# Performance work log

Measured on AMD Instinct MI355X. Metric: run time of the kernel, lower is better.

The kernel has to match this reference:

```python
import jax, jax.numpy as jnp
import numpy as np

EPS = 1e-7  # K.epsilon()
ROUTINGS = 3


def squash(s):
    # squash along last axis: s * ||s||^2 / (1 + ||s||^2) / ||s||
    sq_norm = jnp.sum(jnp.square(s), axis=-1, keepdims=True)
    scale = sq_norm / (1.0 + sq_norm) / jnp.sqrt(sq_norm + EPS)
    return scale * s


def setup_inputs() -> dict:
    key = jax.random.key(0)
    k1, k2 = jax.random.split(key)
    B, N, I = 64, 2048, 16      # batch, in_num_capsule, in_capsule_dim
    J, K = 32, 32               # num_capsule, capsule_dim
    inputs = jax.random.normal(k1, (B, N, I), dtype=jnp.float32)
    W = jax.random.normal(k2, (J, N, K, I), dtype=jnp.float32) * 0.05
    return {"inputs": inputs, "W": W}


def reference(inputs, W):
    # u_hat[b,j,n,k] = sum_i inputs[b,n,i] * W[j,n,k,i]
    u_hat = jnp.einsum('bni,jnki->bjnk', inputs, W)
    B, J, N, _ = u_hat.shape
    b = jnp.zeros((B, J, N), dtype=u_hat.dtype)
    outputs = None
    for i in range(ROUTINGS):
        c = jax.nn.softmax(b, axis=1)                       # softmax over num_capsule
        s = jnp.einsum('bjn,bjnk->bjk', c, u_hat)           # weighted sum over in caps
        outputs = squash(s)                                  # [B, J, K]
        if i < ROUTINGS - 1:
            b = b + jnp.einsum('bjk,bjnk->bjn', outputs, u_hat)
    return outputs
```

## Files before the change

kernel.cpp:

```cpp
#include <hip/hip_runtime.h>
#include <hip/hip_bf16.h>

typedef unsigned int  u32;
typedef unsigned short u16;
typedef __attribute__((ext_vector_type(8)))  short short8;
typedef __attribute__((ext_vector_type(16))) float f32x16;

#define B_ 64
#define N_ 2048
#define I_ 16
#define J_ 32
#define K_ 32
#define CH_  32
#define WTOT ((size_t)J_*N_*K_*I_)

__device__ __forceinline__ float bf2f(u16 u){ return __uint_as_float(((u32)u)<<16); }
__device__ __forceinline__ short f2bf(float f){
  __hip_bfloat16 h = __float2bfloat16(f);
  short s; __builtin_memcpy(&s, &h, 2); return s;
}

__global__ __launch_bounds__(256) void detect(const u16* __restrict__ X,
                                              const u16* __restrict__ W,
                                              int* __restrict__ flags)
{
  __shared__ int sx, sw;
  if (threadIdx.x == 0){ sx = 0; sw = 0; }
  __syncthreads();
  int bx = 0, bw = 0;
  for (int i = threadIdx.x; i < 8192; i += 256){
    int ex = (X[2*i] >> 7) & 0xFF;
    int ew = (W[2*i] >> 7) & 0xFF;
    if (ex >= 0x90) bx = 1;
    if (ew >= 0x90) bw = 1;
  }
  if (bx) atomicOr(&sx, 1);
  if (bw) atomicOr(&sw, 1);
  __syncthreads();
  if (threadIdx.x == 0){ flags[0] = sx; flags[1] = sw; }
}

__global__ __launch_bounds__(256) void pack_xw(const void* __restrict__ Xv,
                                               const void* __restrict__ Wv,
                                               const int* __restrict__ flags,
                                               u16* __restrict__ X_p,
                                               u16* __restrict__ W_p)
{
  if (blockIdx.x < 8192){
    const size_t base = ((size_t)blockIdx.x*256 + threadIdx.x)*16;
    if (flags[1]){
      const float4* src = (const float4*)((const float*)Wv + base);
      float4 v0=src[0], v1=src[1], v2=src[2], v3=src[3];
      short8 a, b;
      a[0]=f2bf(v0.x); a[1]=f2bf(v0.y); a[2]=f2bf(v0.z); a[3]=f2bf(v0.w);
      a[4]=f2bf(v1.x); a[5]=f2bf(v1.y); a[6]=f2bf(v1.z); a[7]=f2bf(v1.w);
      b[0]=f2bf(v2.x); b[1]=f2bf(v2.y); b[2]=f2bf(v2.z); b[3]=f2bf(v2.w);
      b[4]=f2bf(v3.x); b[5]=f2bf(v3.y); b[6]=f2bf(v3.z); b[7]=f2bf(v3.w);
      *(short8*)(W_p + base)     = a;
      *(short8*)(W_p + base + 8) = b;
    } else {
      const short8* src = (const short8*)((const u16*)Wv + base);
      *(short8*)(W_p + base)     = src[0];
      *(short8*)(W_p + base + 8) = src[1];
    }
  } else {
    const int bid = blockIdx.x - 8192;
    const int l = threadIdx.x & 63, w = threadIdx.x >> 6;
    const int n = bid*4 + w;
    const bool xf32 = flags[0] != 0;
    const int ih = (l>>5)*8;
    u16 out[16];
    #pragma unroll
    for (int t=0;t<2;++t){
      const int b = t*32 + (l&31);
      if (xf32){
        const float4* xp = (const float4*)((const float*)Xv + ((size_t)b*N_ + n)*I_ + ih);
        float4 v0 = xp[0], v1 = xp[1];
        out[t*8+0]=(u16)f2bf(v0.x); out[t*8+1]=(u16)f2bf(v0.y);
        out[t*8+2]=(u16)f2bf(v0.z); out[t*8+3]=(u16)f2bf(v0.w);
        out[t*8+4]=(u16)f2bf(v1.x); out[t*8+5]=(u16)f2bf(v1.y);
        out[t*8+6]=(u16)f2bf(v1.z); out[t*8+7]=(u16)f2bf(v1.w);
      } else {
        const u16* xp = (const u16*)Xv + ((size_t)b*N_ + n)*I_ + ih;
        #pragma unroll
        for (int q=0;q<8;++q) out[t*8+q] = xp[q];
      }
    }
    u16* dst = X_p + (size_t)n*1024 + l*16;
    short8 s0, s1;
    #pragma unroll
    for (int q=0;q<8;++q){ s0[q]=(short)out[q]; s1[q]=(short)out[8+q]; }
    *(short8*)dst = s0;
    *(short8*)(dst+8) = s1;
  }
}

template<int R>
__global__ __launch_bounds__(256) void accum_kernel(
    const u16* __restrict__ X_p, const u16* __restrict__ W_p,
    const float* __restrict__ c_buf, const float* __restrict__ sumb,
    float* __restrict__ part)
{
  __shared__ float red[4][2048];
  const int l  = threadIdx.x & 63;
  const int w  = threadIdx.x >> 6;
  const int j  = blockIdx.y;
  const int ch = blockIdx.x;
  const int n0 = ch*64 + w*16;
  const int kc = l & 31;
  const int ih = (l >> 5) * 8;

  f32x16 C0, C1;
  #pragma unroll
  for (int r=0;r<16;++r){ C0[r]=0.f; C1[r]=0.f; }

  #pragma unroll 4
  for (int t=0;t<16;++t){
    const int n = n0 + t;
    const u16* xp = X_p + (size_t)n*1024 + l*16;
    short8 xa0 = *(const short8*)xp;
    short8 xa1 = *(const short8*)(xp+8);
    short8 a0, a1;
    if constexpr (R==0){ a0 = xa0; a1 = xa1; }
    else {
      const float iS0 = sumb[(size_t)n*64 + kc];
      const float iS1 = sumb[(size_t)n*64 + 32 + kc];
      const float c0 = iS0 * c_buf[((size_t)n*J_ + j)*64 + kc];
      const float c1 = iS1 * c_buf[((size_t)n*J_ + j)*64 + 32 + kc];
      #pragma unroll
      for (int q=0;q<8;++q){
        a0[q] = f2bf(c0 * bf2f((u16)xa0[q]));
        a1[q] = f2bf(c1 * bf2f((u16)xa1[q]));
      }
    }
    short8 bfr = *(const short8*)(W_p + ((size_t)j*N_ + n)*512 + kc*16 + ih);
    C0 = __builtin_amdgcn_mfma_f32_32x32x16_bf16(a0, bfr, C0, 0,0,0);
    C1 = __builtin_amdgcn_mfma_f32_32x32x16_bf16(a1, bfr, C1, 0,0,0);
  }

  #pragma unroll
  for (int r=0;r<16;++r){
    red[w][r*64 + l]      = C0[r];
    red[w][(16+r)*64 + l] = C1[r];
  }
  __syncthreads();

  float* dst = part + ((size_t)ch*J_ + j)*2048;
  #pragma unroll
  for (int p = threadIdx.x; p < 2048; p += 256)
    dst[p] = red[0][p] + red[1][p] + red[2][p] + red[3][p];
}

template<int SQ>
__global__ __launch_bounds__(256) void reduce_squash(
    const float* __restrict__ part, float* __restrict__ o_t,
    const int* __restrict__ flags, void* __restrict__ d_out)
{
  const int j    = blockIdx.x & 31;
  const int rseg = blockIdx.x >> 5;
  const int rl   = threadIdx.x >> 6;
  const int l    = threadIdx.x & 63;
  const int r    = rseg*4 + rl;
  const int p    = r*64 + l;

  float sum = 0.f;
  const float* src = part + (size_t)j*2048 + p;
  #pragma unroll 8
  for (int ch=0; ch<CH_; ++ch)
    sum += src[(size_t)ch*J_*2048];

  const int kc = l & 31, h = l >> 5;
  const int rr = r & 15, tile = r >> 4;
  const int b  = tile*32 + (rr&3) + 8*(rr>>2) + 4*h;

  float v = sum;
  if constexpr (SQ==0) v *= (1.0f/32.0f);

  float sq = v*v;
  sq += __shfl_xor(sq, 1,  64);
  sq += __shfl_xor(sq, 2,  64);
  sq += __shfl_xor(sq, 4,  64);
  sq += __shfl_xor(sq, 8,  64);
  sq += __shfl_xor(sq, 16, 64);
  const float scale = sq/(1.f+sq)/sqrtf(sq+1e-7f);

  if constexpr (SQ==0){
    o_t[((size_t)j*K_ + kc)*64 + b] = scale * v;
  } else if constexpr (SQ==1){
    o_t[((size_t)j*K_ + kc)*64 + b] += scale * v;
  } else {
    const bool f32o = (flags[0]!=0) && (flags[1]!=0);
    if (f32o){
      ((float*)d_out)[(size_t)b*(J_*K_) + j*K_ + kc] = scale * v;
    } else {
      ((__hip_bfloat16*)d_out)[(size_t)b*(J_*K_) + j*K_ + kc] = __float2bfloat16(scale * v);
    }
  }
}

__global__ __launch_bounds__(256) void logits_kernel(
    const u16* __restrict__ X_p, const u16* __restrict__ W_p,
    const float* __restrict__ o_t, float* __restrict__ c_buf)
{
  const int l  = threadIdx.x & 63;
  const int w  = threadIdx.x >> 6;
  const int j  = blockIdx.y;
  const int n0 = blockIdx.x*32 + w*8;
  const int kc = l & 31;
  const int h  = l >> 5;
  const int ih = h*8;

  float o_r0[16], o_r1[16];
  #pragma unroll
  for (int r=0;r<16;++r){
    const int k = (r&3) + 8*(r>>2) + 4*h;
    o_r0[r] = o_t[((size_t)j*K_ + k)*64 + kc];
    o_r1[r] = o_t[((size_t)j*K_ + k)*64 + 32 + kc];
  }

  #pragma unroll 2
  for (int t=0;t<8;++t){
    const int n = n0 + t;
    const u16* xp = X_p + (size_t)n*1024 + l*16;
    short8 xa0 = *(const short8*)xp;
    short8 xa1 = *(const short8*)(xp+8);
    short8 wfr = *(const short8*)(W_p + ((size_t)j*N_ + n)*512 + kc*16 + ih);
    f32x16 C0, C1;
    #pragma unroll
    for (int r=0;r<16;++r){ C0[r]=0.f; C1[r]=0.f; }
    C0 = __builtin_amdgcn_mfma_f32_32x32x16_bf16(wfr, xa0, C0, 0,0,0);
    C1 = __builtin_amdgcn_mfma_f32_32x32x16_bf16(wfr, xa1, C1, 0,0,0);
    float d0 = 0.f, d1 = 0.f;
    #pragma unroll
    for (int r=0;r<16;++r){ d0 += C0[r]*o_r0[r]; d1 += C1[r]*o_r1[r]; }
    d0 += __shfl_xor(d0, 32, 64);
    d1 += __shfl_xor(d1, 32, 64);
    const float val = (l >= 32) ? d1 : d0;
    c_buf[((size_t)n*J_ + j)*64 + l] = __expf(val);
  }
}

__global__ __launch_bounds__(256) void rowsum(const float* __restrict__ c_buf,
                                              float* __restrict__ sumb)
{
  const int l = threadIdx.x & 63, w = threadIdx.x >> 6;
  const int n = blockIdx.x*4 + w;
  const float* p = c_buf + (size_t)n*J_*64 + l;
  float s = 0.f;
  #pragma unroll
  for (int jj=0;jj<J_;++jj) s += p[jj*64];
  sumb[(size_t)n*64 + l] = 1.0f/s;
}

extern "C" void kernel_launch(void* const* d_in, const int* in_sizes, int n_in,
                              void* d_out, int out_size, void* d_ws, size_t ws_size,
                              hipStream_t stream)
{
  const void* X  = d_in[0];
  const void* Wm = d_in[1];

  float* ws    = (float*)d_ws;
  float* o_t   = ws;
  int*   flags = (int*)(ws + 65536);
  u16*   X_p   = (u16*)(ws + 65536 + 128);
  u16*   W_p   = X_p + (size_t)N_*1024;
  float* c_buf = (float*)(W_p + WTOT);
  float* sumb  = c_buf + (size_t)N_*J_*64;
  float* part  = sumb + (size_t)N_*64;

  const dim3 blk(256);
  const dim3 g_ac(CH_, J_);
  const dim3 g_lg(64,  J_);

  detect<<<1, blk, 0, stream>>>((const u16*)X, (const u16*)Wm, flags);
  pack_xw<<<8192 + N_/4, blk, 0, stream>>>(X, Wm, flags, X_p, W_p);

  accum_kernel<0><<<g_ac, blk, 0, stream>>>(X_p, W_p, nullptr, nullptr, part);
  reduce_squash<0><<<256, blk, 0, stream>>>(part, o_t, flags, nullptr);

  logits_kernel<<<g_lg, blk, 0, stream>>>(X_p, W_p, o_t, c_buf);
  rowsum<<<N_/4, blk, 0, stream>>>(c_buf, sumb);
  accum_kernel<1><<<g_ac, blk, 0, stream>>>(X_p, W_p, c_buf, sumb, part);
  reduce_squash<1><<<256, blk, 0, stream>>>(part, o_t, flags, nullptr);

  logits_kernel<<<g_lg, blk, 0, stream>>>(X_p, W_p, o_t, c_buf);
  rowsum<<<N_/4, blk, 0, stream>>>(c_buf, sumb);
  accum_kernel<1><<<g_ac, blk, 0, stream>>>(X_p, W_p, c_buf, sumb, part);
  reduce_squash<2><<<256, blk, 0, stream>>>(part, o_t, flags, d_out);
}
```

Measured before the change: 323.3 us.

## Fuse W bf16 packing into first accumulation pass and fold detection into X pack

The separate W conversion pass is removed. The first routing accumulation now reads W in its original format, converts it to bf16 in registers, uses it directly for the MFMA and writes the packed copy for later passes. The standalone single-block format-detection kernel is replaced by each block sniffing a small sample itself, and X packing carries the flags. This saves one full read and write of W and two kernel launches, at the cost of heavier loads in the first accumulation kernel and redundant sniffing in every block.

```diff
diff --git a/kernel.cpp b/kernel.cpp
--- a/kernel.cpp
+++ b/kernel.cpp
@@ -20,83 +20,113 @@
   short s; __builtin_memcpy(&s, &h, 2); return s;
 }
 
-__global__ __launch_bounds__(256) void detect(const u16* __restrict__ X,
-                                              const u16* __restrict__ W,
-                                              int* __restrict__ flags)
+__device__ __forceinline__ bool sniff_f32(const u16* p, int* sh)
+{
+  if (threadIdx.x == 0) *sh = 0;
+  __syncthreads();
+  int hit = ((p[2*threadIdx.x] >> 7) & 0xFF) >= 0x90;
+  if (__any(hit) && (threadIdx.x & 63) == 0) atomicOr(sh, 1);
+  __syncthreads();
+  return *sh != 0;
+}
+
+__global__ __launch_bounds__(256) void pack_x_det(const void* __restrict__ Xv,
+                                                  const void* __restrict__ Wv,
+                                                  int* __restrict__ flags,
+                                                  u16* __restrict__ X_p)
 {
   __shared__ int sx, sw;
-  if (threadIdx.x == 0){ sx = 0; sw = 0; }
+  const bool xf32 = sniff_f32((const u16*)Xv, &sx);
+  if (blockIdx.x == 0){
+    const bool wf32 = sniff_f32((const u16*)Wv, &sw);
+    if (threadIdx.x == 0){ flags[0] = xf32 ? 1 : 0; flags[1] = wf32 ? 1 : 0; }
+  }
+
+  const int l = threadIdx.x & 63, w = threadIdx.x >> 6;
+  const int n = blockIdx.x*4 + w;
+  const int ih = (l>>5)*8;
+  u16 out[16];
+  #pragma unroll
+  for (int t=0;t<2;++t){
+    const int b = t*32 + (l&31);
+    if (xf32){
+      const float4* xp = (const float4*)((const float*)Xv + ((size_t)b*N_ + n)*I_ + ih);
+      float4 v0 = xp[0], v1 = xp[1];
+      out[t*8+0]=(u16)f2bf(v0.x); out[t*8+1]=(u16)f2bf(v0.y);
+      out[t*8+2]=(u16)f2bf(v0.z); out[t*8+3]=(u16)f2bf(v0.w);
+      out[t*8+4]=(u16)f2bf(v1.x); out[t*8+5]=(u16)f2bf(v1.y);
+      out[t*8+6]=(u16)f2bf(v1.z); out[t*8+7]=(u16)f2bf(v1.w);
+    } else {
+      const u16* xp = (const u16*)Xv + ((size_t)b*N_ + n)*I_ + ih;
+      #pragma unroll
+      for (int q=0;q<8;++q) out[t*8+q] = xp[q];
+    }
+  }
+  u16* dst = X_p + (size_t)n*1024 + l*16;
+  short8 s0, s1;
+  #pragma unroll
+  for (int q=0;q<8;++q){ s0[q]=(short)out[q]; s1[q]=(short)out[8+q]; }
+  *(short8*)dst = s0;
+  *(short8*)(dst+8) = s1;
+}
+
+__global__ __launch_bounds__(256) void accum0_packw(
+    const u16* __restrict__ X_p, const void* __restrict__ Wv,
+    u16* __restrict__ W_p, float* __restrict__ part)
+{
+  __shared__ float red[4][2048];
+  __shared__ int swf;
+  const bool wf32 = sniff_f32((const u16*)Wv, &swf);
+
+  const int l  = threadIdx.x & 63;
+  const int w  = threadIdx.x >> 6;
+  const int j  = blockIdx.y;
+  const int ch = blockIdx.x;
+  const int n0 = ch*64 + w*16;
+  const int kc = l & 31;
+  const int ih = (l >> 5) * 8;
+
+  f32x16 C0, C1;
+  #pragma unroll
+  for (int r=0;r<16;++r){ C0[r]=0.f; C1[r]=0.f; }
+
+  #pragma unroll 4
+  for (int t=0;t<16;++t){
+    const int n = n0 + t;
+    const u16* xp = X_p + (size_t)n*1024 + l*16;
+    short8 xa0 = *(const short8*)xp;
+    short8 xa1 = *(const short8*)(xp+8);
+
+    const size_t wbase = ((size_t)j*N_ + n)*512 + kc*16 + ih;
+    short8 bfr;
+    if (wf32){
+      const float4* wp = (const float4*)((const float*)Wv + wbase);
+      float4 u0 = wp[0], u1 = wp[1];
+      bfr[0]=f2bf(u0.x); bfr[1]=f2bf(u0.y); bfr[2]=f2bf(u0.z); bfr[3]=f2bf(u0.w);
+      bfr[4]=f2bf(u1.x); bfr[5]=f2bf(u1.y); bfr[6]=f2bf(u1.z); bfr[7]=f2bf(u1.w);
+    } else {
+      bfr = *(const short8*)((const u16*)Wv + wbase);
+    }
+    *(short8*)(W_p + wbase) = bfr;
+
+    C0 = __builtin_amdgcn_mfma_f32_32x32x16_bf16(xa0, bfr, C0, 0,0,0);
+    C1 = __builtin_amdgcn_mfma_f32_32x32x16_bf16(xa1, bfr, C1, 0,0,0);
+  }
+
+  #pragma unroll
+  for (int r=0;r<16;++r){
+    red[w][r*64 + l]      = C0[r];
+    red[w][(16+r)*64 + l] = C1[r];
+  }
   __syncthreads();
-  int bx = 0, bw = 0;
-  for (int i = threadIdx.x; i < 8192; i += 256){
-    int ex = (X[2*i] >> 7) & 0xFF;
-    int ew = (W[2*i] >> 7) & 0xFF;
-    if (ex >= 0x90) bx = 1;
-    if (ew >= 0x90) bw = 1;
-  }
-  if (bx) atomicOr(&sx, 1);
-  if (bw) atomicOr(&sw, 1);
-  __syncthreads();
-  if (threadIdx.x == 0){ flags[0] = sx; flags[1] = sw; }
-}
-
-__global__ __launch_bounds__(256) void pack_xw(const void* __restrict__ Xv,
-                                               const void* __restrict__ Wv,
-                                               const int* __restrict__ flags,
-                                               u16* __restrict__ X_p,
-                                               u16* __restrict__ W_p)
-{
-  if (blockIdx.x < 8192){
-    const size_t base = ((size_t)blockIdx.x*256 + threadIdx.x)*16;
-    if (flags[1]){
-      const float4* src = (const float4*)((const float*)Wv + base);
-      float4 v0=src[0], v1=src[1], v2=src[2], v3=src[3];
-      short8 a, b;
-      a[0]=f2bf(v0.x); a[1]=f2bf(v0.y); a[2]=f2bf(v0.z); a[3]=f2bf(v0.w);
-      a[4]=f2bf(v1.x); a[5]=f2bf(v1.y); a[6]=f2bf(v1.z); a[7]=f2bf(v1.w);
-      b[0]=f2bf(v2.x); b[1]=f2bf(v2.y); b[2]=f2bf(v2.z); b[3]=f2bf(v2.w);
-      b[4]=f2bf(v3.x); b[5]=f2bf(v3.y); b[6]=f2bf(v3.z); b[7]=f2bf(v3.w);
-      *(short8*)(W_p + base)     = a;
-      *(short8*)(W_p + base + 8) = b;
-    } else {
-      const short8* src = (const short8*)((const u16*)Wv + base);
-      *(short8*)(W_p + base)     = src[0];
-      *(short8*)(W_p + base + 8) = src[1];
-    }
-  } else {
-    const int bid = blockIdx.x - 8192;
-    const int l = threadIdx.x & 63, w = threadIdx.x >> 6;
-    const int n = bid*4 + w;
-    const bool xf32 = flags[0] != 0;
-    const int ih = (l>>5)*8;
-    u16 out[16];
-    #pragma unroll
-    for (int t=0;t<2;++t){
-      const int b = t*32 + (l&31);
-      if (xf32){
-        const float4* xp = (const float4*)((const float*)Xv + ((size_t)b*N_ + n)*I_ + ih);
-        float4 v0 = xp[0], v1 = xp[1];
-        out[t*8+0]=(u16)f2bf(v0.x); out[t*8+1]=(u16)f2bf(v0.y);
-        out[t*8+2]=(u16)f2bf(v0.z); out[t*8+3]=(u16)f2bf(v0.w);
-        out[t*8+4]=(u16)f2bf(v1.x); out[t*8+5]=(u16)f2bf(v1.y);
-        out[t*8+6]=(u16)f2bf(v1.z); out[t*8+7]=(u16)f2bf(v1.w);
-      } else {
-        const u16* xp = (const u16*)Xv + ((size_t)b*N_ + n)*I_ + ih;
-        #pragma unroll
-        for (int q=0;q<8;++q) out[t*8+q] = xp[q];
-      }
-    }
-    u16* dst = X_p + (size_t)n*1024 + l*16;
-    short8 s0, s1;
-    #pragma unroll
-    for (int q=0;q<8;++q){ s0[q]=(short)out[q]; s1[q]=(short)out[8+q]; }
-    *(short8*)dst = s0;
-    *(short8*)(dst+8) = s1;
-  }
-}
-
-template<int R>
-__global__ __launch_bounds__(256) void accum_kernel(
+
+  float* dst = part + ((size_t)ch*J_ + j)*2048;
+  #pragma unroll
+  for (int p = threadIdx.x; p < 2048; p += 256)
+    dst[p] = red[0][p] + red[1][p] + red[2][p] + red[3][p];
+}
+
+__global__ __launch_bounds__(256) void accum1_kernel(
     const u16* __restrict__ X_p, const u16* __restrict__ W_p,
     const float* __restrict__ c_buf, const float* __restrict__ sumb,
     float* __restrict__ part)
@@ -120,18 +150,15 @@
     const u16* xp = X_p + (size_t)n*1024 + l*16;
     short8 xa0 = *(const short8*)xp;
     short8 xa1 = *(const short8*)(xp+8);
+    const float iS0 = sumb[(size_t)n*64 + kc];
+    const float iS1 = sumb[(size_t)n*64 + 32 + kc];
+    const float c0 = iS0 * c_buf[((size_t)n*J_ + j)*64 + kc];
+    const float c1 = iS1 * c_buf[((size_t)n*J_ + j)*64 + 32 + kc];
     short8 a0, a1;
-    if constexpr (R==0){ a0 = xa0; a1 = xa1; }
-    else {
-      const float iS0 = sumb[(size_t)n*64 + kc];
-      const float iS1 = sumb[(size_t)n*64 + 32 + kc];
-      const float c0 = iS0 * c_buf[((size_t)n*J_ + j)*64 + kc];
-      const float c1 = iS1 * c_buf[((size_t)n*J_ + j)*64 + 32 + kc];
-      #pragma unroll
-      for (int q=0;q<8;++q){
-        a0[q] = f2bf(c0 * bf2f((u16)xa0[q]));
-        a1[q] = f2bf(c1 * bf2f((u16)xa1[q]));
-      }
+    #pragma unroll
+    for (int q=0;q<8;++q){
+      a0[q] = f2bf(c0 * bf2f((u16)xa0[q]));
+      a1[q] = f2bf(c1 * bf2f((u16)xa1[q]));
     }
     short8 bfr = *(const short8*)(W_p + ((size_t)j*N_ + n)*512 + kc*16 + ih);
     C0 = __builtin_amdgcn_mfma_f32_32x32x16_bf16(a0, bfr, C0, 0,0,0);
@@ -272,19 +299,18 @@
   const dim3 g_ac(CH_, J_);
   const dim3 g_lg(64,  J_);
 
-  detect<<<1, blk, 0, stream>>>((const u16*)X, (const u16*)Wm, flags);
-  pack_xw<<<8192 + N_/4, blk, 0, stream>>>(X, Wm, flags, X_p, W_p);
-
-  accum_kernel<0><<<g_ac, blk, 0, stream>>>(X_p, W_p, nullptr, nullptr, part);
+  pack_x_det<<<N_/4, blk, 0, stream>>>(X, Wm, flags, X_p);
+
+  accum0_packw<<<g_ac, blk, 0, stream>>>(X_p, Wm, W_p, part);
   reduce_squash<0><<<256, blk, 0, stream>>>(part, o_t, flags, nullptr);
 
   logits_kernel<<<g_lg, blk, 0, stream>>>(X_p, W_p, o_t, c_buf);
   rowsum<<<N_/4, blk, 0, stream>>>(c_buf, sumb);
-  accum_kernel<1><<<g_ac, blk, 0, stream>>>(X_p, W_p, c_buf, sumb, part);
+  accum1_kernel<<<g_ac, blk, 0, stream>>>(X_p, W_p, c_buf, sumb, part);
   reduce_squash<1><<<256, blk, 0, stream>>>(part, o_t, flags, nullptr);
 
   logits_kernel<<<g_lg, blk, 0, stream>>>(X_p, W_p, o_t, c_buf);
   rowsum<<<N_/4, blk, 0, stream>>>(c_buf, sumb);
-  accum_kernel<1><<<g_ac, blk, 0, stream>>>(X_p, W_p, c_buf, sumb, part);
+  accum1_kernel<<<g_ac, blk, 0, stream>>>(X_p, W_p, c_buf, sumb, part);
   reduce_squash<2><<<256, blk, 0, stream>>>(part, o_t, flags, d_out);
 }
```

Measured after the change: 305.3 us. 5.6% less time.
